# Performance work log

Hardware: AMD Instinct MI355X
Metric: run time of the kernel (lower is better)

## Reference

```python
import jax, jax.numpy as jnp
import numpy as np

B, S, D = 8, 512, 512
H = 8
DPH = D // H
FFN = 2048
N_LAYERS = 4
K = 2048 * 8  # vocab_size * vq_vocab_size_factor
COMMIT = 0.25
LN_EPS = 1e-5
# replicates torch bug: scale = key.size(-1)//num_heads AFTER head split view
SCALE = DPH // H  # 64 // 8 = 8, attention is MULTIPLIED by this


def setup_inputs():
    key = jax.random.key(0)
    ks = jax.random.split(key, 12)
    init = lambda k, shape, s=0.02: (jax.random.normal(k, shape, jnp.float32) * s)
    inp = {
        'vec_inputs': jax.random.normal(ks[0], (B, S, D), jnp.float32),
        'Wq': init(ks[1], (N_LAYERS, D, D)), 'bq': jnp.zeros((N_LAYERS, D)),
        'Wk': init(ks[2], (N_LAYERS, D, D)), 'bk': jnp.zeros((N_LAYERS, D)),
        'Wv': init(ks[3], (N_LAYERS, D, D)), 'bv': jnp.zeros((N_LAYERS, D)),
        'Wo': init(ks[4], (N_LAYERS, D, D)), 'bo': jnp.zeros((N_LAYERS, D)),
        'ln1_g': jnp.ones((N_LAYERS, D)), 'ln1_b': jnp.zeros((N_LAYERS, D)),
        'W1': init(ks[5], (N_LAYERS, D, FFN)), 'b1': jnp.zeros((N_LAYERS, FFN)),
        'W2': init(ks[6], (N_LAYERS, FFN, D)), 'b2': jnp.zeros((N_LAYERS, D)),
        'ln2_g': jnp.ones((N_LAYERS, D)), 'ln2_b': jnp.zeros((N_LAYERS, D)),
        # VectorQuantizerEMA: embedding.weight.data.normal_()
        'codebook': jax.random.normal(ks[7], (K, D), jnp.float32),
    }
    return inp


def _layernorm(x, g, b):
    mu = jnp.mean(x, axis=-1, keepdims=True)
    var = jnp.mean((x - mu) ** 2, axis=-1, keepdims=True)
    return (x - mu) * jax.lax.rsqrt(var + LN_EPS) * g + b


def _encoder_layer(x, Wq, bq, Wk, bk, Wv, bv, Wo, bo, ln1_g, ln1_b, W1, b1, W2, b2, ln2_g, ln2_b):
    resid = x
    q = x @ Wq + bq  # [B,S,D]
    k = x @ Wk + bk
    v = x @ Wv + bv
    # faithful to torch .view(B*H, -1, dph): raw row-major reshape (NOT transpose split)
    q = q.reshape(B * H, S, DPH)
    k = k.reshape(B * H, S, DPH)
    v = v.reshape(B * H, S, DPH)
    att = jnp.einsum('bqd,bkd->bqk', q, k) * SCALE
    att = jax.nn.softmax(att, axis=-1)
    ctx = jnp.einsum('bqk,bkd->bqd', att, v).reshape(B, S, D)
    out = ctx @ Wo + bo
    out = _layernorm(resid + out, ln1_g, ln1_b)
    # position-wise FFN (Conv1d kernel 1 == Linear)
    ff = jax.nn.relu(out @ W1 + b1) @ W2 + b2
    out = _layernorm(out + ff, ln2_g, ln2_b)
    return out


def reference(vec_inputs, Wq, bq, Wk, bk, Wv, bv, Wo, bo, ln1_g, ln1_b,
              W1, b1, W2, b2, ln2_g, ln2_b, codebook):
    ze = vec_inputs
    for l in range(N_LAYERS):
        ze = _encoder_layer(ze, Wq[l], bq[l], Wk[l], bk[l], Wv[l], bv[l], Wo[l], bo[l],
                            ln1_g[l], ln1_b[l], W1[l], b1[l], W2[l], b2[l], ln2_g[l], ln2_b[l])
    # VectorQuantizerEMA forward (eval mode: no EMA updates)
    flat = ze.reshape(-1, D)  # [B*S, D]
    d = (jnp.sum(flat ** 2, axis=1, keepdims=True)
         + jnp.sum(codebook ** 2, axis=1)
         - 2.0 * flat @ codebook.T)  # [B*S, K]
    idx = jnp.argmin(d, axis=1)  # [B*S]
    quant = codebook[idx].reshape(ze.shape)
    e_latent = jnp.mean((jax.lax.stop_gradient(quant) - ze) ** 2)
    loss = COMMIT * e_latent
    zq = ze + jax.lax.stop_gradient(quant - ze)  # straight-through
    avg_probs = jnp.zeros((K,), jnp.float32).at[idx].add(1.0) / flat.shape[0]
    perplexity = jnp.exp(-jnp.sum(avg_probs * jnp.log(avg_probs + 1e-10)))
    return zq, idx.reshape(B, S), loss, perplexity
```

## Files before the change

kernel.cpp:

```cpp
#include <hip/hip_runtime.h>

#define MROWS 4096
#define DDIM  512
#define FFND  2048
#define NLAY  4
#define KCB   16384
#define LN_EPS 1e-5f

typedef unsigned short u16;
typedef _Float16 half8 __attribute__((ext_vector_type(8)));
typedef float f32x4 __attribute__((ext_vector_type(4)));

#define B_X    0ULL
#define B_Q    8388608ULL
#define B_K    16777216ULL
#define B_V    25165824ULL
#define B_CT   33554432ULL
#define B_TMP  41943040ULL
#define B_H    8388608ULL
#define B_CBH  8388608ULL
#define B_CBL  25165824ULL
#define B_ZEH  41943040ULL
#define B_ZEL  46137344ULL
#define B_ZN   50331648ULL
#define B_CN   50348032ULL
#define B_RL   50413568ULL
#define B_BEST 50429952ULL
#define B_HIST 50462720ULL
#define B_WT   50528256ULL

__device__ __forceinline__ void splitf16(float x, u16& h, u16& l) {
  _Float16 hh = (_Float16)x;
  float r = x - (float)hh;
  _Float16 ll = (_Float16)r;
  h = *(u16*)&hh; l = *(u16*)&ll;
}

__device__ __forceinline__ unsigned int fkey(float f) {
  unsigned int u = __float_as_uint(f);
  return (u & 0x80000000u) ? ~u : (u | 0x80000000u);
}

template<int EPI>
__device__ __forceinline__ void gemm64_body(const float* __restrict__ Af,
    const u16* __restrict__ Bhi, const u16* __restrict__ Blo,
    const float* __restrict__ bias, float* __restrict__ C, int Kd, int N) {
  __shared__ __align__(16) u16 As[2][2048];
  __shared__ __align__(16) u16 Bs[2][4096];
  const int t = threadIdx.x;
  const int w = t >> 6, l = t & 63;
  const int lr = l & 15, lg = l >> 4;
  const int m0 = blockIdx.y * 64, n0 = blockIdx.x * 128;

  f32x4 acc[4][2];
  const f32x4 zf = {0.f, 0.f, 0.f, 0.f};
#pragma unroll
  for (int mi = 0; mi < 4; ++mi)
#pragma unroll
    for (int ni = 0; ni < 2; ++ni) acc[mi][ni] = zf;

  for (int k0 = 0; k0 < Kd; k0 += 32) {
#pragma unroll
    for (int pl = 0; pl < 2; ++pl) {
      const u16* gp = pl ? Blo : Bhi;
      u16* lb = &Bs[pl][0];
#pragma unroll
      for (int i = 0; i < 2; ++i) {
        int ob = w * 2048 + i * 1024;
        int o = ob + l * 16;
        int r = o >> 6;
        int pc = (o >> 4) & 3;
        int c = pc ^ ((r + (r >> 2)) & 3);
        const u16* g = gp + (size_t)(n0 + r) * Kd + k0 + c * 8;
        __builtin_amdgcn_global_load_lds(
            (const __attribute__((address_space(1))) unsigned int*)(const void*)g,
            (__attribute__((address_space(3))) unsigned int*)(void*)(lb + (ob >> 1)), 16, 0, 0);
      }
    }
#pragma unroll
    for (int p = 0; p < 2; ++p) {
      int e = p * 256 + t;
      int r = e >> 3, kc = (e & 7) * 4;
      float4 a = *(const float4*)(Af + (size_t)(m0 + r) * Kd + k0 + kc);
      u16 h0, h1, h2, h3, q0, q1, q2, q3;
      splitf16(a.x, h0, q0); splitf16(a.y, h1, q1); splitf16(a.z, h2, q2); splitf16(a.w, h3, q3);
      int idx = r * 32 + ((((kc >> 3) ^ ((r + (r >> 2)) & 3))) << 3) + (kc & 7);
      *(uint2*)&As[0][idx] = make_uint2((unsigned)h0 | ((unsigned)h1 << 16), (unsigned)h2 | ((unsigned)h3 << 16));
      *(uint2*)&As[1][idx] = make_uint2((unsigned)q0 | ((unsigned)q1 << 16), (unsigned)q2 | ((unsigned)q3 << 16));
    }
    __syncthreads();
    half8 ah[4], al[4], bh2[2], bl2[2];
#pragma unroll
    for (int mi = 0; mi < 4; ++mi) {
      int r = mi * 16 + lr;
      int idx = r * 32 + ((lg ^ ((r + (r >> 2)) & 3)) << 3);
      ah[mi] = *(const half8*)&As[0][idx];
      al[mi] = *(const half8*)&As[1][idx];
    }
#pragma unroll
    for (int ni = 0; ni < 2; ++ni) {
      int r = w * 32 + ni * 16 + lr;
      int idx = r * 32 + ((lg ^ ((r + (r >> 2)) & 3)) << 3);
      bh2[ni] = *(const half8*)&Bs[0][idx];
      bl2[ni] = *(const half8*)&Bs[1][idx];
    }
#pragma unroll
    for (int mi = 0; mi < 4; ++mi)
#pragma unroll
      for (int ni = 0; ni < 2; ++ni) {
        acc[mi][ni] = __builtin_amdgcn_mfma_f32_16x16x32_f16(ah[mi], bh2[ni], acc[mi][ni], 0, 0, 0);
        acc[mi][ni] = __builtin_amdgcn_mfma_f32_16x16x32_f16(ah[mi], bl2[ni], acc[mi][ni], 0, 0, 0);
        acc[mi][ni] = __builtin_amdgcn_mfma_f32_16x16x32_f16(al[mi], bh2[ni], acc[mi][ni], 0, 0, 0);
      }
    __syncthreads();
  }

  float bv[2];
#pragma unroll
  for (int ni = 0; ni < 2; ++ni) bv[ni] = bias[n0 + w * 32 + ni * 16 + lr];
#pragma unroll
  for (int mi = 0; mi < 4; ++mi)
#pragma unroll
    for (int j = 0; j < 4; ++j) {
      int m = m0 + mi * 16 + lg * 4 + j;
#pragma unroll
      for (int ni = 0; ni < 2; ++ni) {
        int n = n0 + w * 32 + ni * 16 + lr;
        float o = acc[mi][ni][j] + bv[ni];
        if (EPI == 1) o = fmaxf(o, 0.f);
        C[(size_t)m * N + n] = o;
      }
    }
}

__global__ __launch_bounds__(256) void gemm_enc(const float* __restrict__ Af,
    const u16* __restrict__ Bhi, const u16* __restrict__ Blo,
    const float* __restrict__ bias, float* __restrict__ C, int Kd, int N) {
  gemm64_body<0>(Af, Bhi, Blo, bias, C, Kd, N);
}

__global__ __launch_bounds__(256) void qkv_enc(const float* __restrict__ Af,
    const u16* __restrict__ wt, const float* __restrict__ bq, const float* __restrict__ bk,
    const float* __restrict__ bv_, float* __restrict__ Cq) {
  const int z = blockIdx.z;
  const u16* Bhi = wt + (size_t)z * 524288;
  const u16* Blo = Bhi + 262144;
  const float* bias = (z == 0) ? bq : (z == 1) ? bk : bv_;
  float* C = Cq + (size_t)z * 2097152;
  gemm64_body<0>(Af, Bhi, Blo, bias, C, 512, 512);
}

template<int EPI>
__global__ __launch_bounds__(256) void gemm128(const float* __restrict__ Af,
    const u16* __restrict__ Bhi, const u16* __restrict__ Blo,
    const float* __restrict__ bias, float* __restrict__ C, int Kd, int N) {
  __shared__ __align__(16) u16 As[2][4096];
  __shared__ __align__(16) u16 Bs[2][4096];
  const int t = threadIdx.x;
  const int w = t >> 6, l = t & 63;
  const int lr = l & 15, lg = l >> 4;
  const int wr = w >> 1, wc = w & 1;
  const int m0 = blockIdx.y * 128, n0 = blockIdx.x * 128;

  f32x4 acc[4][4];
  const f32x4 zf = {0.f, 0.f, 0.f, 0.f};
#pragma unroll
  for (int mi = 0; mi < 4; ++mi)
#pragma unroll
    for (int ni = 0; ni < 4; ++ni) acc[mi][ni] = zf;

  for (int k0 = 0; k0 < Kd; k0 += 32) {
#pragma unroll
    for (int pl = 0; pl < 2; ++pl) {
      const u16* gp = pl ? Blo : Bhi;
      u16* lb = &Bs[pl][0];
#pragma unroll
      for (int i = 0; i < 2; ++i) {
        int ob = (w * 2 + i) * 1024;
        int o = ob + l * 16;
        int r = o >> 6;
        int c = ((o >> 4) & 3) ^ ((r + (r >> 2)) & 3);
        const u16* g = gp + (size_t)(n0 + r) * Kd + k0 + c * 8;
        __builtin_amdgcn_global_load_lds(
            (const __attribute__((address_space(1))) unsigned int*)(const void*)g,
            (__attribute__((address_space(3))) unsigned int*)(void*)(lb + (ob >> 1)), 16, 0, 0);
      }
    }
#pragma unroll
    for (int p = 0; p < 4; ++p) {
      int e = p * 256 + t;
      int r = e >> 3, kc = (e & 7) * 4;
      float4 a = *(const float4*)(Af + (size_t)(m0 + r) * Kd + k0 + kc);
      u16 h0, h1, h2, h3, q0, q1, q2, q3;
      splitf16(a.x, h0, q0); splitf16(a.y, h1, q1); splitf16(a.z, h2, q2); splitf16(a.w, h3, q3);
      int idx = r * 32 + ((((kc >> 3) ^ ((r + (r >> 2)) & 3))) << 3) + (kc & 7);
      *(uint2*)&As[0][idx] = make_uint2((unsigned)h0 | ((unsigned)h1 << 16), (unsigned)h2 | ((unsigned)h3 << 16));
      *(uint2*)&As[1][idx] = make_uint2((unsigned)q0 | ((unsigned)q1 << 16), (unsigned)q2 | ((unsigned)q3 << 16));
    }
    __syncthreads();
    half8 ah[4], al[4], bh4[4], bl4[4];
#pragma unroll
    for (int mi = 0; mi < 4; ++mi) {
      int r = wr * 64 + mi * 16 + lr;
      int idx = r * 32 + ((lg ^ ((r + (r >> 2)) & 3)) << 3);
      ah[mi] = *(const half8*)&As[0][idx];
      al[mi] = *(const half8*)&As[1][idx];
    }
#pragma unroll
    for (int ni = 0; ni < 4; ++ni) {
      int r = wc * 64 + ni * 16 + lr;
      int idx = r * 32 + ((lg ^ ((r + (r >> 2)) & 3)) << 3);
      bh4[ni] = *(const half8*)&Bs[0][idx];
      bl4[ni] = *(const half8*)&Bs[1][idx];
    }
#pragma unroll
    for (int mi = 0; mi < 4; ++mi)
#pragma unroll
      for (int ni = 0; ni < 4; ++ni) {
        acc[mi][ni] = __builtin_amdgcn_mfma_f32_16x16x32_f16(ah[mi], bh4[ni], acc[mi][ni], 0, 0, 0);
        acc[mi][ni] = __builtin_amdgcn_mfma_f32_16x16x32_f16(ah[mi], bl4[ni], acc[mi][ni], 0, 0, 0);
        acc[mi][ni] = __builtin_amdgcn_mfma_f32_16x16x32_f16(al[mi], bh4[ni], acc[mi][ni], 0, 0, 0);
      }
    __syncthreads();
  }

  float bv[4];
#pragma unroll
  for (int ni = 0; ni < 4; ++ni) bv[ni] = bias[n0 + wc * 64 + ni * 16 + lr];
#pragma unroll
  for (int mi = 0; mi < 4; ++mi)
#pragma unroll
    for (int j = 0; j < 4; ++j) {
      int m = m0 + wr * 64 + mi * 16 + lg * 4 + j;
#pragma unroll
      for (int ni = 0; ni < 4; ++ni) {
        int n = n0 + wc * 64 + ni * 16 + lr;
        float o = acc[mi][ni][j] + bv[ni];
        if (EPI == 1) o = fmaxf(o, 0.f);
        C[(size_t)m * N + n] = o;
      }
    }
}

__global__ __launch_bounds__(512) void attn_mfma(const float* __restrict__ Q,
    const float* __restrict__ Kx, const float* __restrict__ V, float* __restrict__ O) {
  __shared__ __align__(16) u16 Ks[2][4608];
  __shared__ __align__(16) u16 Ps[2][9216];
  __shared__ __align__(16) u16 Vt[2][4608];
  const int t = threadIdx.x;
  const int w = t >> 6, l = t & 63;
  const int lr = l & 15, lg = l >> 4;
  const int bh = blockIdx.y;
  const int q0 = blockIdx.x * 128;
  const float* Qb = Q + ((size_t)bh * 512 + q0) * 64;
  const float* Kb = Kx + (size_t)bh * 512 * 64;
  const float* Vb = V + (size_t)bh * 512 * 64;

  half8 qh[2], qlo[2];
#pragma unroll
  for (int ks = 0; ks < 2; ++ks) {
    const float* p = Qb + (size_t)(w * 16 + lr) * 64 + ks * 32 + lg * 8;
    float4 f0 = *(const float4*)p;
    float4 f1 = *(const float4*)(p + 4);
    float v8[8] = {f0.x, f0.y, f0.z, f0.w, f1.x, f1.y, f1.z, f1.w};
#pragma unroll
    for (int j = 0; j < 8; ++j) {
      _Float16 hh = (_Float16)v8[j];
      float r = v8[j] - (float)hh;
      qh[ks][j] = hh;
      qlo[ks][j] = (_Float16)r;
    }
  }

  float mrun[4] = {-1e30f, -1e30f, -1e30f, -1e30f};
  float lrun[4] = {0.f, 0.f, 0.f, 0.f};
  f32x4 o[4];
  const f32x4 zf = {0.f, 0.f, 0.f, 0.f};
#pragma unroll
  for (int dn = 0; dn < 4; ++dn) o[dn] = zf;

#pragma unroll 1
  for (int kc = 0; kc < 8; ++kc) {
    __syncthreads();
#pragma unroll
    for (int i = 0; i < 2; ++i) {
      int e = i * 512 + t;
      int row = e >> 4, c4 = (e & 15) * 4;
      float4 kv4 = *(const float4*)(Kb + (size_t)(kc * 64 + row) * 64 + c4);
      u16 h0, h1, h2, h3, l0, l1, l2, l3;
      splitf16(kv4.x, h0, l0); splitf16(kv4.y, h1, l1); splitf16(kv4.z, h2, l2); splitf16(kv4.w, h3, l3);
      *(uint2*)&Ks[0][row * 72 + c4] = make_uint2((unsigned)h0 | ((unsigned)h1 << 16), (unsigned)h2 | ((unsigned)h3 << 16));
      *(uint2*)&Ks[1][row * 72 + c4] = make_uint2((unsigned)l0 | ((unsigned)l1 << 16), (unsigned)l2 | ((unsigned)l3 << 16));
      float4 vv4 = *(const float4*)(Vb + (size_t)(kc * 64 + row) * 64 + c4);
      u16 vh[4], vl[4];
      splitf16(vv4.x, vh[0], vl[0]); splitf16(vv4.y, vh[1], vl[1]);
      splitf16(vv4.z, vh[2], vl[2]); splitf16(vv4.w, vh[3], vl[3]);
#pragma unroll
      for (int ii = 0; ii < 4; ++ii) {
        Vt[0][(c4 + ii) * 72 + row] = vh[ii];
        Vt[1][(c4 + ii) * 72 + row] = vl[ii];
      }
    }
    __syncthreads();
    f32x4 sa[4];
#pragma unroll
    for (int ni = 0; ni < 4; ++ni) sa[ni] = zf;
    __builtin_amdgcn_s_setprio(1);
#pragma unroll
    for (int ks = 0; ks < 2; ++ks) {
#pragma unroll
      for (int ni = 0; ni < 4; ++ni) {
        half8 kh = *(const half8*)&Ks[0][(ni * 16 + lr) * 72 + ks * 32 + lg * 8];
        half8 klo = *(const half8*)&Ks[1][(ni * 16 + lr) * 72 + ks * 32 + lg * 8];
        sa[ni] = __builtin_amdgcn_mfma_f32_16x16x32_f16(qh[ks], kh, sa[ni], 0, 0, 0);
        sa[ni] = __builtin_amdgcn_mfma_f32_16x16x32_f16(qh[ks], klo, sa[ni], 0, 0, 0);
        sa[ni] = __builtin_amdgcn_mfma_f32_16x16x32_f16(qlo[ks], kh, sa[ni], 0, 0, 0);
      }
    }
    __builtin_amdgcn_s_setprio(0);
#pragma unroll
    for (int j = 0; j < 4; ++j) {
      float sv[4];
#pragma unroll
      for (int ni = 0; ni < 4; ++ni) sv[ni] = sa[ni][j] * 8.f;
      float mx = fmaxf(fmaxf(sv[0], sv[1]), fmaxf(sv[2], sv[3]));
#pragma unroll
      for (int off = 8; off; off >>= 1) mx = fmaxf(mx, __shfl_xor(mx, off, 16));
      float mnew = fmaxf(mrun[j], mx);
      float fac = expf(mrun[j] - mnew);
      float ps = 0.f;
#pragma unroll
      for (int ni = 0; ni < 4; ++ni) {
        float p = expf(sv[ni] - mnew);
        ps += p;
        u16 ph_, pl_;
        splitf16(p, ph_, pl_);
        Ps[0][(w * 16 + lg * 4 + j) * 72 + ni * 16 + lr] = ph_;
        Ps[1][(w * 16 + lg * 4 + j) * 72 + ni * 16 + lr] = pl_;
      }
#pragma unroll
      for (int off = 8; off; off >>= 1) ps += __shfl_xor(ps, off, 16);
      lrun[j] = lrun[j] * fac + ps;
      mrun[j] = mnew;
#pragma unroll
      for (int dn = 0; dn < 4; ++dn) o[dn][j] *= fac;
    }
    __builtin_amdgcn_s_setprio(1);
#pragma unroll
    for (int ks = 0; ks < 2; ++ks) {
      half8 ph8 = *(const half8*)&Ps[0][(w * 16 + lr) * 72 + ks * 32 + lg * 8];
      half8 pl8 = *(const half8*)&Ps[1][(w * 16 + lr) * 72 + ks * 32 + lg * 8];
#pragma unroll
      for (int dn = 0; dn < 4; ++dn) {
        half8 vh8 = *(const half8*)&Vt[0][(dn * 16 + lr) * 72 + ks * 32 + lg * 8];
        half8 vl8 = *(const half8*)&Vt[1][(dn * 16 + lr) * 72 + ks * 32 + lg * 8];
        o[dn] = __builtin_amdgcn_mfma_f32_16x16x32_f16(ph8, vh8, o[dn], 0, 0, 0);
        o[dn] = __builtin_amdgcn_mfma_f32_16x16x32_f16(ph8, vl8, o[dn], 0, 0, 0);
        o[dn] = __builtin_amdgcn_mfma_f32_16x16x32_f16(pl8, vh8, o[dn], 0, 0, 0);
      }
    }
    __builtin_amdgcn_s_setprio(0);
  }
  float inv[4];
#pragma unroll
  for (int j = 0; j < 4; ++j) inv[j] = 1.f / lrun[j];
  float* Ob = O + ((size_t)bh * 512 + q0) * 64;
#pragma unroll
  for (int dn = 0; dn < 4; ++dn)
#pragma unroll
    for (int j = 0; j < 4; ++j)
      Ob[(size_t)(w * 16 + lg * 4 + j) * 64 + dn * 16 + lr] = o[dn][j] * inv[j];
}

__global__ __launch_bounds__(1024) void vq256(
    const u16* __restrict__ Ahi, const u16* __restrict__ Alo,
    const u16* __restrict__ Bhi, const u16* __restrict__ Blo,
    const float* __restrict__ zn, const float* __restrict__ cn,
    unsigned long long* __restrict__ best) {
  __shared__ __align__(16) u16 As[2][2][8192];
  __shared__ __align__(16) u16 Bs[2][2][8192];
  const int t = threadIdx.x;
  const int w = t >> 6, l = t & 63;
  const int lr = l & 15, lg = l >> 4;
  const int wr = w >> 2, wc = w & 3;
  const int f = blockIdx.x;
  const int xcd = f & 7, pos = f >> 3;
  const int ml = pos & 15;
  const int nl = pos >> 4;
  const int n0 = (xcd * 8 + nl) * 256;
  const int m0 = ml * 256;

  f32x4 acc[4][4];
  const f32x4 zf = {0.f, 0.f, 0.f, 0.f};
#pragma unroll
  for (int mi = 0; mi < 4; ++mi)
#pragma unroll
    for (int ni = 0; ni < 4; ++ni) acc[mi][ni] = zf;

  const int s_ob = w * 1024;
  int s_r, s_c;
  {
    int o = s_ob + l * 16;
    s_r = o >> 6;
    s_c = ((o >> 4) & 3) ^ ((s_r + (s_r >> 2)) & 3);
  }

#define VQ_STAGE(buf, k0)                                                               \
  {                                                                                     \
    size_t ea = (size_t)(m0 + s_r) * 512 + (k0) + s_c * 8;                              \
    size_t eb = (size_t)(n0 + s_r) * 512 + (k0) + s_c * 8;                              \
    __builtin_amdgcn_global_load_lds(                                                   \
        (const __attribute__((address_space(1))) unsigned int*)(const void*)(Ahi + ea), \
        (__attribute__((address_space(3))) unsigned int*)(void*)(&As[buf][0][s_ob >> 1]), 16, 0, 0); \
    __builtin_amdgcn_global_load_lds(                                                   \
        (const __attribute__((address_space(1))) unsigned int*)(const void*)(Alo + ea), \
        (__attribute__((address_space(3))) unsigned int*)(void*)(&As[buf][1][s_ob >> 1]), 16, 0, 0); \
    __builtin_amdgcn_global_load_lds(                                                   \
        (const __attribute__((address_space(1))) unsigned int*)(const void*)(Bhi + eb), \
        (__attribute__((address_space(3))) unsigned int*)(void*)(&Bs[buf][0][s_ob >> 1]), 16, 0, 0); \
    __builtin_amdgcn_global_load_lds(                                                   \
        (const __attribute__((address_space(1))) unsigned int*)(const void*)(Blo + eb), \
        (__attribute__((address_space(3))) unsigned int*)(void*)(&Bs[buf][1][s_ob >> 1]), 16, 0, 0); \
  }

#define VQ_COMPUTE(buf)                                                                 \
  {                                                                                     \
    half8 bh[4], bl[4];                                                                 \
    _Pragma("unroll")                                                                   \
    for (int ni = 0; ni < 4; ++ni) {                                                    \
      int r = wc * 64 + ni * 16 + lr;                                                   \
      int idx = r * 32 + ((lg ^ ((r + (r >> 2)) & 3)) << 3);                            \
      bh[ni] = *(const half8*)&Bs[buf][0][idx];                                         \
      bl[ni] = *(const half8*)&Bs[buf][1][idx];                                         \
    }                                                                                   \
    _Pragma("unroll")                                                                   \
    for (int mi = 0; mi < 4; ++mi) {                                                    \
      int r = wr * 64 + mi * 16 + lr;                                                   \
      int idx = r * 32 + ((lg ^ ((r + (r >> 2)) & 3)) << 3);                            \
      half8 ah = *(const half8*)&As[buf][0][idx];                                       \
      half8 al = *(const half8*)&As[buf][1][idx];                                       \
      _Pragma("unroll")                                                                 \
      for (int ni = 0; ni < 4; ++ni) {                                                  \
        acc[mi][ni] = __builtin_amdgcn_mfma_f32_16x16x32_f16(ah, bh[ni], acc[mi][ni], 0, 0, 0); \
        acc[mi][ni] = __builtin_amdgcn_mfma_f32_16x16x32_f16(ah, bl[ni], acc[mi][ni], 0, 0, 0); \
        acc[mi][ni] = __builtin_amdgcn_mfma_f32_16x16x32_f16(al, bh[ni], acc[mi][ni], 0, 0, 0); \
      }                                                                                 \
    }                                                                                   \
  }

  VQ_STAGE(0, 0);
  asm volatile("s_waitcnt vmcnt(0)" ::: "memory");
  __builtin_amdgcn_s_barrier();
  int cur = 0;
#pragma unroll 1
  for (int ks = 0; ks < 16; ++ks) {
    if (ks < 15) VQ_STAGE(cur ^ 1, (ks + 1) * 32);
    VQ_COMPUTE(cur);
    asm volatile("s_waitcnt vmcnt(0)" ::: "memory");
    __builtin_amdgcn_s_barrier();
    cur ^= 1;
  }

  float cnv[4];
#pragma unroll
  for (int ni = 0; ni < 4; ++ni) cnv[ni] = cn[n0 + wc * 64 + ni * 16 + lr];
#pragma unroll
  for (int mi = 0; mi < 4; ++mi)
#pragma unroll
    for (int j = 0; j < 4; ++j) {
      int m = m0 + wr * 64 + mi * 16 + lg * 4 + j;
      float zr = zn[m];
      float db = 3.4e38f; int jb = 0;
#pragma unroll
      for (int ni = 0; ni < 4; ++ni) {
        float dd = zr + cnv[ni] - 2.f * acc[mi][ni][j];
        int nn = n0 + wc * 64 + ni * 16 + lr;
        if (dd < db) { db = dd; jb = nn; }
      }
      unsigned long long key = ((unsigned long long)fkey(db) << 32) | (unsigned int)jb;
#pragma unroll
      for (int off = 8; off; off >>= 1) {
        unsigned long long o = __shfl_xor(key, off, 16);
        if (o < key) key = o;
      }
      if (lr == 0) atomicMin(best + m, key);
    }
#undef VQ_STAGE
#undef VQ_COMPUTE
}

__global__ __launch_bounds__(256) void wcvt_layer(const float* __restrict__ Wq,
    const float* __restrict__ Wk, const float* __restrict__ Wv, const float* __restrict__ Wo,
    const float* __restrict__ W1, const float* __restrict__ W2, u16* __restrict__ wt) {
  __shared__ float Ls[64][68];
  const int T = blockIdx.x, t = threadIdx.x;
  const float* src; u16 *dh, *dl; int K, N, kt, nt;
  if (T < 256) {
    int mat = T >> 6, tt = T & 63;
    src = (mat == 0) ? Wq : (mat == 1) ? Wk : (mat == 2) ? Wv : Wo;
    dh = wt + (size_t)mat * 524288; dl = dh + 262144;
    K = 512; N = 512; kt = tt >> 3; nt = tt & 7;
  } else if (T < 512) {
    int tt = T - 256; src = W1; dh = wt + 2097152; dl = dh + 1048576;
    K = 512; N = 2048; kt = tt >> 5; nt = tt & 31;
  } else {
    int tt = T - 512; src = W2; dh = wt + 4194304; dl = dh + 1048576;
    K = 2048; N = 512; kt = tt >> 3; nt = tt & 7;
  }
  const int k0 = kt * 64, n0 = nt * 64;
#pragma unroll
  for (int p = 0; p < 4; ++p) {
    int e = p * 256 + t;
    int kr = e >> 4, nc = (e & 15) * 4;
    *(float4*)&Ls[kr][nc] = *(const float4*)(src + (size_t)(k0 + kr) * N + n0 + nc);
  }
  __syncthreads();
  {
    int n = t >> 2, kc = (t & 3) * 16;
    unsigned hw[8], lw[8];
#pragma unroll
    for (int i = 0; i < 8; ++i) {
      u16 ha, la, hb, lb;
      splitf16(Ls[kc + 2 * i][n], ha, la);
      splitf16(Ls[kc + 2 * i + 1][n], hb, lb);
      hw[i] = (unsigned)ha | ((unsigned)hb << 16);
      lw[i] = (unsigned)la | ((unsigned)lb << 16);
    }
    size_t o = (size_t)(n0 + n) * K + k0 + kc;
    *(uint4*)&dh[o] = make_uint4(hw[0], hw[1], hw[2], hw[3]);
    *(uint4*)&dh[o + 8] = make_uint4(hw[4], hw[5], hw[6], hw[7]);
    *(uint4*)&dl[o] = make_uint4(lw[0], lw[1], lw[2], lw[3]);
    *(uint4*)&dl[o + 8] = make_uint4(lw[4], lw[5], lw[6], lw[7]);
  }
}

__global__ __launch_bounds__(128) void zcvt_kernel(const float* __restrict__ src,
    u16* __restrict__ hi, u16* __restrict__ lo, float* __restrict__ nrm) {
  __shared__ float red[2];
  const int row = blockIdx.x, t = threadIdx.x;
  const float4 a = *(const float4*)(src + (size_t)row * 512 + t * 4);
  u16 h0, h1, h2, h3, q0, q1, q2, q3;
  splitf16(a.x, h0, q0); splitf16(a.y, h1, q1); splitf16(a.z, h2, q2); splitf16(a.w, h3, q3);
  *(uint2*)&hi[(size_t)row * 512 + t * 4] = make_uint2((unsigned)h0 | ((unsigned)h1 << 16), (unsigned)h2 | ((unsigned)h3 << 16));
  *(uint2*)&lo[(size_t)row * 512 + t * 4] = make_uint2((unsigned)q0 | ((unsigned)q1 << 16), (unsigned)q2 | ((unsigned)q3 << 16));
  float s = a.x * a.x + a.y * a.y + a.z * a.z + a.w * a.w;
#pragma unroll
  for (int off = 32; off; off >>= 1) s += __shfl_xor(s, off, 64);
  if ((t & 63) == 0) red[t >> 6] = s;
  __syncthreads();
  if (t == 0) nrm[row] = red[0] + red[1];
}

__global__ __launch_bounds__(128) void ln_kernel(const float* __restrict__ A,
    const float* __restrict__ Dl, const float* __restrict__ g,
    const float* __restrict__ bb, float* __restrict__ out) {
  __shared__ float red[2];
  const int row = blockIdx.x, t = threadIdx.x;
  const float4 a = *(const float4*)(A + (size_t)row * 512 + t * 4);
  const float4 d = *(const float4*)(Dl + (size_t)row * 512 + t * 4);
  float v0 = a.x + d.x, v1 = a.y + d.y, v2 = a.z + d.z, v3 = a.w + d.w;
  float s = v0 + v1 + v2 + v3;
#pragma unroll
  for (int off = 32; off; off >>= 1) s += __shfl_xor(s, off, 64);
  if ((t & 63) == 0) red[t >> 6] = s;
  __syncthreads();
  const float mu = (red[0] + red[1]) * (1.f / 512.f);
  const float w0 = v0 - mu, w1 = v1 - mu, w2 = v2 - mu, w3 = v3 - mu;
  float q = w0 * w0 + w1 * w1 + w2 * w2 + w3 * w3;
  __syncthreads();
#pragma unroll
  for (int off = 32; off; off >>= 1) q += __shfl_xor(q, off, 64);
  if ((t & 63) == 0) red[t >> 6] = q;
  __syncthreads();
  const float rs = rsqrtf((red[0] + red[1]) * (1.f / 512.f) + LN_EPS);
  const float4 gv = *(const float4*)(g + t * 4);
  const float4 bv = *(const float4*)(bb + t * 4);
  *(float4*)(out + (size_t)row * 512 + t * 4) =
      make_float4(w0 * rs * gv.x + bv.x, w1 * rs * gv.y + bv.y, w2 * rs * gv.z + bv.z, w3 * rs * gv.w + bv.w);
}

__global__ __launch_bounds__(128) void gather_kernel(const unsigned long long* __restrict__ best,
    const float* __restrict__ Cb, const float* __restrict__ Ze, float* __restrict__ zq,
    float* __restrict__ oidx, float* __restrict__ rloss, int* __restrict__ hist) {
  __shared__ float red[2];
  const int row = blockIdx.x, t = threadIdx.x;
  const int idx = (int)(best[row] & 0xFFFFFFFFULL);
  const float4 c = *(const float4*)(Cb + (size_t)idx * 512 + t * 4);
  const float4 z = *(const float4*)(Ze + (size_t)row * 512 + t * 4);
  *(float4*)(zq + (size_t)row * 512 + t * 4) = c;
  const float d0 = c.x - z.x, d1 = c.y - z.y, d2 = c.z - z.z, d3 = c.w - z.w;
  float s = d0 * d0 + d1 * d1 + d2 * d2 + d3 * d3;
#pragma unroll
  for (int off = 32; off; off >>= 1) s += __shfl_xor(s, off, 64);
  if ((t & 63) == 0) red[t >> 6] = s;
  __syncthreads();
  if (t == 0) {
    rloss[row] = red[0] + red[1];
    oidx[row] = (float)idx;
    atomicAdd(hist + idx, 1);
  }
}

__global__ __launch_bounds__(256) void fin_kernel(const float* __restrict__ rloss,
    const int* __restrict__ hist, float* __restrict__ oloss, float* __restrict__ oppl) {
  __shared__ float red[4];
  const int t = threadIdx.x;
  float s = 0.f;
  for (int i = t; i < 4096; i += 256) s += rloss[i];
#pragma unroll
  for (int off = 32; off; off >>= 1) s += __shfl_xor(s, off, 64);
  if ((t & 63) == 0) red[t >> 6] = s;
  __syncthreads();
  if (t == 0) oloss[0] = 0.25f * (red[0] + red[1] + red[2] + red[3]) * (1.f / 2097152.f);
  float e = 0.f;
  for (int i = t; i < KCB; i += 256) {
    float p = (float)hist[i] * (1.f / 4096.f);
    e += p * logf(p + 1e-10f);
  }
#pragma unroll
  for (int off = 32; off; off >>= 1) e += __shfl_xor(e, off, 64);
  __syncthreads();
  if ((t & 63) == 0) red[t >> 6] = e;
  __syncthreads();
  if (t == 0) oppl[0] = expf(-(red[0] + red[1] + red[2] + red[3]));
}

extern "C" void kernel_launch(void* const* d_in, const int* in_sizes, int n_in,
                              void* d_out, int out_size, void* d_ws, size_t ws_size,
                              hipStream_t stream) {
  const float* vec  = (const float*)d_in[0];
  const float* Wq   = (const float*)d_in[1];
  const float* bq   = (const float*)d_in[2];
  const float* Wk   = (const float*)d_in[3];
  const float* bk   = (const float*)d_in[4];
  const float* Wv   = (const float*)d_in[5];
  const float* bv   = (const float*)d_in[6];
  const float* Wo   = (const float*)d_in[7];
  const float* bo   = (const float*)d_in[8];
  const float* l1g  = (const float*)d_in[9];
  const float* l1b  = (const float*)d_in[10];
  const float* W1   = (const float*)d_in[11];
  const float* b1   = (const float*)d_in[12];
  const float* W2   = (const float*)d_in[13];
  const float* b2   = (const float*)d_in[14];
  const float* l2g  = (const float*)d_in[15];
  const float* l2b  = (const float*)d_in[16];
  const float* cb   = (const float*)d_in[17];

  char* wsb = (char*)d_ws;
  float* x   = (float*)(wsb + B_X);
  float* q   = (float*)(wsb + B_Q);
  float* k   = (float*)(wsb + B_K);
  float* v   = (float*)(wsb + B_V);
  float* ctx = (float*)(wsb + B_CT);
  float* tmp = (float*)(wsb + B_TMP);
  float* h   = (float*)(wsb + B_H);
  u16* cbh = (u16*)(wsb + B_CBH);
  u16* cbl = (u16*)(wsb + B_CBL);
  u16* zeh = (u16*)(wsb + B_ZEH);
  u16* zel = (u16*)(wsb + B_ZEL);
  float* zn = (float*)(wsb + B_ZN);
  float* cn = (float*)(wsb + B_CN);
  float* rl = (float*)(wsb + B_RL);
  unsigned long long* best = (unsigned long long*)(wsb + B_BEST);
  int* hist = (int*)(wsb + B_HIST);
  u16* wt = (u16*)(wsb + B_WT);
  u16* wto_h = wt + 1572864;      u16* wto_l = wt + 1835008;
  u16* wt1_h = wt + 2097152;      u16* wt1_l = wt + 3145728;
  u16* wt2_h = wt + 4194304;      u16* wt2_l = wt + 5242880;

  float* zq   = (float*)d_out;
  float* oidx = (float*)d_out + 2097152;
  float* olos = (float*)d_out + 2097152 + 4096;
  float* oppl = olos + 1;

  const dim3 gQkv(4, 64, 3);
  const dim3 gProj(4, 64);
  const dim3 gFfn1(16, 32);
  const dim3 gAttn(4, 64);

  for (int l = 0; l < NLAY; ++l) {
    const float* xin = l ? (const float*)x : vec;
    const size_t wo = (size_t)l * DDIM * DDIM;
    wcvt_layer<<<768, 256, 0, stream>>>(Wq + wo, Wk + wo, Wv + wo, Wo + wo,
        W1 + (size_t)l * DDIM * FFND, W2 + (size_t)l * FFND * DDIM, wt);
    qkv_enc<<<gQkv, 256, 0, stream>>>(xin, wt, bq + l * DDIM, bk + l * DDIM, bv + l * DDIM, q);
    attn_mfma<<<gAttn, 512, 0, stream>>>(q, k, v, ctx);
    gemm_enc<<<gProj, 256, 0, stream>>>(ctx, wto_h, wto_l, bo + l * DDIM, tmp, DDIM, DDIM);
    ln_kernel<<<MROWS, 128, 0, stream>>>(xin, tmp, l1g + l * DDIM, l1b + l * DDIM, x);
    gemm128<1><<<gFfn1, 256, 0, stream>>>(x, wt1_h, wt1_l, b1 + l * FFND, h, DDIM, FFND);
    gemm_enc<<<gProj, 256, 0, stream>>>(h, wt2_h, wt2_l, b2 + l * DDIM, tmp, FFND, DDIM);
    ln_kernel<<<MROWS, 128, 0, stream>>>(x, tmp, l2g + l * DDIM, l2b + l * DDIM, x);
  }

  zcvt_kernel<<<MROWS, 128, 0, stream>>>(x, zeh, zel, zn);
  zcvt_kernel<<<KCB, 128, 0, stream>>>(cb, cbh, cbl, cn);
  hipMemsetAsync(best, 0xFF, 4096 * 8, stream);
  hipMemsetAsync(hist, 0, KCB * 4, stream);
  vq256<<<1024, 1024, 0, stream>>>(zeh, zel, cbh, cbl, zn, cn, best);
  gather_kernel<<<MROWS, 128, 0, stream>>>(best, cb, x, zq, oidx, rl, hist);
  fin_kernel<<<1, 256, 0, stream>>>(rl, hist, olos, oppl);
}
```

Baseline: 1.042 ms.

## Add double-buffered pipelined GEMM for output projection and FFN2

Replaces the generic gemm_enc used for the attention output projection and the second FFN matmul with a new kernel. The new kernel double-buffers the A and B tiles in LDS and issues the next k-slice's global loads (async global_load_lds for B, register prefetch for A) before the current slice's MFMAs. The goal is to hide global memory latency behind compute. It roughly doubles LDS use and raises register pressure, which may cut occupancy.

```diff
diff --git a/kernel.cpp b/kernel.cpp
--- a/kernel.cpp
+++ b/kernel.cpp
@@ -133,12 +133,6 @@
     }
 }
 
-__global__ __launch_bounds__(256) void gemm_enc(const float* __restrict__ Af,
-    const u16* __restrict__ Bhi, const u16* __restrict__ Blo,
-    const float* __restrict__ bias, float* __restrict__ C, int Kd, int N) {
-  gemm64_body<0>(Af, Bhi, Blo, bias, C, Kd, N);
-}
-
 __global__ __launch_bounds__(256) void qkv_enc(const float* __restrict__ Af,
     const u16* __restrict__ wt, const float* __restrict__ bq, const float* __restrict__ bk,
     const float* __restrict__ bv_, float* __restrict__ Cq) {
@@ -148,6 +142,136 @@
   const float* bias = (z == 0) ? bq : (z == 1) ? bk : bv_;
   float* C = Cq + (size_t)z * 2097152;
   gemm64_body<0>(Af, Bhi, Blo, bias, C, 512, 512);
+}
+
+template<int EPI>
+__global__ __launch_bounds__(256) void gemm_enc_p(const float* __restrict__ Af,
+    const u16* __restrict__ Bhi, const u16* __restrict__ Blo,
+    const float* __restrict__ bias, float* __restrict__ C, int Kd, int N) {
+  __shared__ __align__(16) u16 As[2][2][2048];
+  __shared__ __align__(16) u16 Bs[2][2][4096];
+  const int t = threadIdx.x;
+  const int w = t >> 6, l = t & 63;
+  const int lr = l & 15, lg = l >> 4;
+  const int m0 = blockIdx.y * 64, n0 = blockIdx.x * 128;
+
+  f32x4 acc[4][2];
+  const f32x4 zf = {0.f, 0.f, 0.f, 0.f};
+#pragma unroll
+  for (int mi = 0; mi < 4; ++mi)
+#pragma unroll
+    for (int ni = 0; ni < 2; ++ni) acc[mi][ni] = zf;
+
+  int b_ob[2], b_r[2], b_c[2];
+#pragma unroll
+  for (int i = 0; i < 2; ++i) {
+    int ob = w * 2048 + i * 1024;
+    int o = ob + l * 16;
+    int r = o >> 6;
+    int c = ((o >> 4) & 3) ^ ((r + (r >> 2)) & 3);
+    b_ob[i] = ob; b_r[i] = r; b_c[i] = c;
+  }
+  int a_r[2], a_kc[2], a_idx[2];
+#pragma unroll
+  for (int p = 0; p < 2; ++p) {
+    int e = p * 256 + t;
+    a_r[p] = e >> 3; a_kc[p] = (e & 7) * 4;
+    a_idx[p] = a_r[p] * 32 + ((((a_kc[p] >> 3) ^ ((a_r[p] + (a_r[p] >> 2)) & 3))) << 3) + (a_kc[p] & 7);
+  }
+
+#define GP_STAGE_B(buf, k0)                                                             \
+  { _Pragma("unroll")                                                                   \
+    for (int pl = 0; pl < 2; ++pl) {                                                    \
+      const u16* gp = pl ? Blo : Bhi;                                                   \
+      _Pragma("unroll")                                                                 \
+      for (int i = 0; i < 2; ++i) {                                                     \
+        const u16* g = gp + (size_t)(n0 + b_r[i]) * Kd + (k0) + b_c[i] * 8;             \
+        __builtin_amdgcn_global_load_lds(                                               \
+            (const __attribute__((address_space(1))) unsigned int*)(const void*)g,      \
+            (__attribute__((address_space(3))) unsigned int*)(void*)(&Bs[buf][pl][b_ob[i] >> 1]), 16, 0, 0); \
+      } } }
+
+#define GP_LOAD_A(ar, k0)                                                               \
+  { _Pragma("unroll")                                                                   \
+    for (int p = 0; p < 2; ++p)                                                         \
+      ar[p] = *(const float4*)(Af + (size_t)(m0 + a_r[p]) * Kd + (k0) + a_kc[p]); }
+
+#define GP_WRITE_A(buf, ar)                                                             \
+  { _Pragma("unroll")                                                                   \
+    for (int p = 0; p < 2; ++p) {                                                       \
+      u16 h0, h1, h2, h3, q0, q1, q2, q3;                                               \
+      splitf16(ar[p].x, h0, q0); splitf16(ar[p].y, h1, q1);                             \
+      splitf16(ar[p].z, h2, q2); splitf16(ar[p].w, h3, q3);                             \
+      *(uint2*)&As[buf][0][a_idx[p]] = make_uint2((unsigned)h0 | ((unsigned)h1 << 16), (unsigned)h2 | ((unsigned)h3 << 16)); \
+      *(uint2*)&As[buf][1][a_idx[p]] = make_uint2((unsigned)q0 | ((unsigned)q1 << 16), (unsigned)q2 | ((unsigned)q3 << 16)); \
+    } }
+
+  {
+    float4 a0[2];
+    GP_LOAD_A(a0, 0);
+    GP_STAGE_B(0, 0);
+    GP_WRITE_A(0, a0);
+  }
+  asm volatile("s_waitcnt vmcnt(0) lgkmcnt(0)" ::: "memory");
+  __builtin_amdgcn_s_barrier();
+
+  int cur = 0;
+  const int nk = Kd >> 5;
+#pragma unroll 1
+  for (int ks = 0; ks < nk; ++ks) {
+    half8 ah[4], al[4], bh2[2], bl2[2];
+#pragma unroll
+    for (int mi = 0; mi < 4; ++mi) {
+      int r = mi * 16 + lr;
+      int idx = r * 32 + ((lg ^ ((r + (r >> 2)) & 3)) << 3);
+      ah[mi] = *(const half8*)&As[cur][0][idx];
+      al[mi] = *(const half8*)&As[cur][1][idx];
+    }
+#pragma unroll
+    for (int ni = 0; ni < 2; ++ni) {
+      int r = w * 32 + ni * 16 + lr;
+      int idx = r * 32 + ((lg ^ ((r + (r >> 2)) & 3)) << 3);
+      bh2[ni] = *(const half8*)&Bs[cur][0][idx];
+      bl2[ni] = *(const half8*)&Bs[cur][1][idx];
+    }
+    float4 an[2];
+    if (ks + 1 < nk) {
+      GP_LOAD_A(an, (ks + 1) * 32);
+      GP_STAGE_B(cur ^ 1, (ks + 1) * 32);
+    }
+#pragma unroll
+    for (int mi = 0; mi < 4; ++mi)
+#pragma unroll
+      for (int ni = 0; ni < 2; ++ni) {
+        acc[mi][ni] = __builtin_amdgcn_mfma_f32_16x16x32_f16(ah[mi], bh2[ni], acc[mi][ni], 0, 0, 0);
+        acc[mi][ni] = __builtin_amdgcn_mfma_f32_16x16x32_f16(ah[mi], bl2[ni], acc[mi][ni], 0, 0, 0);
+        acc[mi][ni] = __builtin_amdgcn_mfma_f32_16x16x32_f16(al[mi], bh2[ni], acc[mi][ni], 0, 0, 0);
+      }
+    if (ks + 1 < nk) GP_WRITE_A(cur ^ 1, an);
+    asm volatile("s_waitcnt vmcnt(0) lgkmcnt(0)" ::: "memory");
+    __builtin_amdgcn_s_barrier();
+    cur ^= 1;
+  }
+
+  float bv[2];
+#pragma unroll
+  for (int ni = 0; ni < 2; ++ni) bv[ni] = bias[n0 + w * 32 + ni * 16 + lr];
+#pragma unroll
+  for (int mi = 0; mi < 4; ++mi)
+#pragma unroll
+    for (int j = 0; j < 4; ++j) {
+      int m = m0 + mi * 16 + lg * 4 + j;
+#pragma unroll
+      for (int ni = 0; ni < 2; ++ni) {
+        int n = n0 + w * 32 + ni * 16 + lr;
+        float o = acc[mi][ni][j] + bv[ni];
+        if (EPI == 1) o = fmaxf(o, 0.f);
+        C[(size_t)m * N + n] = o;
+      }
+    }
+#undef GP_STAGE_B
+#undef GP_LOAD_A
+#undef GP_WRITE_A
 }
 
 template<int EPI>
@@ -686,10 +810,10 @@
         W1 + (size_t)l * DDIM * FFND, W2 + (size_t)l * FFND * DDIM, wt);
     qkv_enc<<<gQkv, 256, 0, stream>>>(xin, wt, bq + l * DDIM, bk + l * DDIM, bv + l * DDIM, q);
     attn_mfma<<<gAttn, 512, 0, stream>>>(q, k, v, ctx);
-    gemm_enc<<<gProj, 256, 0, stream>>>(ctx, wto_h, wto_l, bo + l * DDIM, tmp, DDIM, DDIM);
+    gemm_enc_p<0><<<gProj, 256, 0, stream>>>(ctx, wto_h, wto_l, bo + l * DDIM, tmp, DDIM, DDIM);
     ln_kernel<<<MROWS, 128, 0, stream>>>(xin, tmp, l1g + l * DDIM, l1b + l * DDIM, x);
     gemm128<1><<<gFfn1, 256, 0, stream>>>(x, wt1_h, wt1_l, b1 + l * FFND, h, DDIM, FFND);
-    gemm_enc<<<gProj, 256, 0, stream>>>(h, wt2_h, wt2_l, b2 + l * DDIM, tmp, FFND, DDIM);
+    gemm_enc_p<0><<<gProj, 256, 0, stream>>>(h, wt2_h, wt2_l, b2 + l * DDIM, tmp, FFND, DDIM);
     ln_kernel<<<MROWS, 128, 0, stream>>>(x, tmp, l2g + l * DDIM, l2b + l * DDIM, x);
   }
 
```

Result: no change. 1.043 ms (+0.1%).
